# Kernel optimization log

Measured on AMD Instinct MI355X. Metric: run time of the kernel, lower is better.

## Reference

```python
import jax, jax.numpy as jnp
import numpy as np

D_MODEL = 2048
D_STATE = 16
D_CONV = 4
EXPAND = 2
D_INNER = EXPAND * D_MODEL  # 4096
BATCH = 32768


def setup_inputs() -> dict:
    key = jax.random.key(0)
    ks = jax.random.split(key, 8)
    x = jax.random.normal(ks[0], (BATCH, D_MODEL), dtype=jnp.float32)
    in_w = jax.random.normal(ks[1], (D_MODEL, D_INNER), dtype=jnp.float32) * 0.02
    in_b = jnp.zeros((D_INNER,), jnp.float32)
    # depthwise conv kernel: (d_inner, d_conv) (groups == channels, so in-chan dim is 1)
    conv_w = jax.random.normal(ks[2], (D_INNER, D_CONV), dtype=jnp.float32) * 0.1
    conv_b = jnp.zeros((D_INNER,), jnp.float32)
    # A = log(arange(1, d_state+1)) broadcast to (d_inner, d_state), as in __init__
    A_log = jnp.log(jnp.broadcast_to(
        jnp.arange(1, D_STATE + 1, dtype=jnp.float32), (D_INNER, D_STATE)))
    B = jax.random.normal(ks[3], (D_INNER, D_STATE), dtype=jnp.float32)
    C = jax.random.normal(ks[4], (D_INNER, D_STATE), dtype=jnp.float32)
    Dp = jnp.ones((D_INNER,), jnp.float32)
    dt = jnp.ones((D_INNER,), jnp.float32)
    out_w = jax.random.normal(ks[5], (D_INNER, D_MODEL), dtype=jnp.float32) * 0.02
    out_b = jnp.zeros((D_MODEL,), jnp.float32)
    return dict(x=x, in_w=in_w, in_b=in_b, conv_w=conv_w, conv_b=conv_b,
                A_log=A_log, B=B, C=C, Dp=Dp, dt=dt, out_w=out_w, out_b=out_b)


def reference(x, in_w, in_b, conv_w, conv_b, A_log, B, C, Dp, dt, out_w, out_b):
    # in_proj: (batch, d_model) -> (batch, d_inner)
    xi = x @ in_w + in_b

    # Depthwise causal Conv1d(kernel=d_conv, padding=d_conv-1) on a length-1
    # sequence; torch takes x_conv[:, :, :1]. Output position 0 sees (d_conv-1)
    # left-pad zeros followed by x, so only the LAST kernel tap contributes:
    x_conv = xi * conv_w[:, -1] + conv_b  # (batch, d_inner)

    # Single-step selective scan with zero initial state:
    #   delta = softplus(dt);  A = -exp(A_log)
    #   h = exp(delta*A) * h0 + delta * B * u  (h0 = 0 => exp term vanishes)
    #   y = sum_n C[:,n] * h[:,:,n] + D * u
    # which reduces per-channel to: y = u * (delta * sum_n(B*C) + D)
    delta = jax.nn.softplus(dt)                       # (d_inner,)
    A = -jnp.exp(A_log)                               # (d_inner, d_state) (cancels with h0=0)
    del A
    bc = jnp.sum(B * C, axis=-1)                      # (d_inner,)
    y = xi * (delta * bc + Dp)                        # (batch, d_inner)

    out = jax.nn.silu(x_conv + y)                     # SiLU gate
    return out @ out_w + out_b                        # (batch, d_model)
```

## Files before the change

kernel.cpp:

```cpp
#include <hip/hip_runtime.h>
#include <stdint.h>
#include <stddef.h>

#define D_MODEL 2048
#define D_INNER 4096

typedef float f32x4 __attribute__((ext_vector_type(4)));
typedef short short8 __attribute__((ext_vector_type(8)));
typedef __bf16 bf16x8 __attribute__((ext_vector_type(8)));

static __device__ __forceinline__ unsigned short f32_to_bf16(float f){
  unsigned int u = __builtin_bit_cast(unsigned int, f);
  u += 0x7FFFu + ((u >> 16) & 1u);
  return (unsigned short)(u >> 16);
}

static __device__ __forceinline__ f32x4 mfma_bf16(short8 a, short8 b, f32x4 c){
  return __builtin_amdgcn_mfma_f32_16x16x32_bf16(
      __builtin_bit_cast(bf16x8, a), __builtin_bit_cast(bf16x8, b), c, 0, 0, 0);
}

static __device__ __forceinline__ void gload_lds16(const void* g, void* l){
  __builtin_amdgcn_global_load_lds(
      (const __attribute__((address_space(1))) void*)g,
      (__attribute__((address_space(3))) void*)l, 16, 0, 0);
}

__global__ void prep_coef_k(const float* __restrict__ conv_w, const float* __restrict__ Bm,
                            const float* __restrict__ Cm, const float* __restrict__ Dp,
                            const float* __restrict__ dt, float* __restrict__ coef){
  int c = blockIdx.x * 256 + threadIdx.x;
  if (c >= D_INNER) return;
  float d = dt[c];
  float sp = (d > 20.f) ? d : log1pf(__expf(d));
  float bc = 0.f;
  #pragma unroll
  for (int n = 0; n < 16; n++) bc += Bm[c*16+n] * Cm[c*16+n];
  coef[c] = conv_w[c*4+3] + sp * bc + Dp[c];
}

__global__ void transpose_cvt_k(const float* __restrict__ in, unsigned short* __restrict__ outT,
                                int K, int N){
  __shared__ float t[32][33];
  int n0 = blockIdx.x * 32, k0 = blockIdx.y * 32;
  int tx = threadIdx.x, ty = threadIdx.y;
  #pragma unroll
  for (int i = 0; i < 4; i++)
    t[ty + 8*i][tx] = in[(size_t)(k0 + ty + 8*i) * N + n0 + tx];
  __syncthreads();
  #pragma unroll
  for (int i = 0; i < 4; i++)
    outT[(size_t)(n0 + ty + 8*i) * K + k0 + tx] = f32_to_bf16(t[tx][ty + 8*i]);
}

__global__ void cvt_x_k(const float4* __restrict__ x, ushort4* __restrict__ xb, int n4){
  int stride = gridDim.x * blockDim.x;
  for (int i = blockIdx.x * blockDim.x + threadIdx.x; i < n4; i += stride){
    float4 v = x[i];
    ushort4 o;
    o.x = f32_to_bf16(v.x); o.y = f32_to_bf16(v.y);
    o.z = f32_to_bf16(v.z); o.w = f32_to_bf16(v.w);
    xb[i] = o;
  }
}

template<int EPI>
__global__ __launch_bounds__(512, 2) void gemm8_k(
    const unsigned short* __restrict__ A,
    const unsigned short* __restrict__ Bt,
    int M, int N, int K,
    const float* __restrict__ bias,
    const float* __restrict__ coef,
    const float* __restrict__ convb,
    unsigned short* __restrict__ gate,
    float* __restrict__ out)
{
  __shared__ __align__(16) unsigned short smem[65536];
  char* ldsc = (char*)smem;

  const int tid = threadIdx.x;
  const int wid = tid >> 6, lane = tid & 63;
  const int wr = wid >> 2, wc = wid & 3;
  const int l15 = lane & 15, lg = lane >> 4;

  const int nbx = N >> 8;
  const int cpx = gridDim.x >> 3;
  const int bid = blockIdx.x;
  const int swz = (bid & 7) * cpx + (bid >> 3);
  const int m0 = (swz / nbx) << 8, n0 = (swz % nbx) << 8;

  const int cswz = lg ^ ((l15 >> 1) & 3);
  const int aoff = (wr*128 + l15)*64 + cswz*16;
  const int boff = (wc*64  + l15)*64 + cswz*16;

  const int s0 = wid*128 + lane;
  const int s1 = s0 + 64;
  const int r0 = s0 >> 2, r1 = s1 >> 2;
  const int c0 = (s0 & 3) ^ ((r0 >> 1) & 3);
  const int c1 = (s1 & 3) ^ ((r1 >> 1) & 3);
  const unsigned short* pA0 = A  + (size_t)(m0 + r0)*K + c0*8;
  const unsigned short* pA1 = A  + (size_t)(m0 + r1)*K + c1*8;
  const unsigned short* pB0 = Bt + (size_t)(n0 + r0)*K + c0*8;
  const unsigned short* pB1 = Bt + (size_t)(n0 + r1)*K + c1*8;

  const int ntile = K >> 6;

#define STAGE_(ST, SKS, SMAT) do {                                          \
    int st_ = (ST); if (st_ > ntile-1) st_ = ntile-1;                       \
    const int ktks_ = st_*64 + (SKS)*32;                                    \
    unsigned short* reg_ = smem + ((st_ & 1) << 15) + ((SMAT) << 14) + ((SKS) << 13); \
    if ((SMAT) == 0) {                                                      \
      gload_lds16(pA0 + ktks_, reg_ + s0*8);                                \
      gload_lds16(pA1 + ktks_, reg_ + s1*8);                                \
    } else {                                                                \
      gload_lds16(pB0 + ktks_, reg_ + s0*8);                                \
      gload_lds16(pB1 + ktks_, reg_ + s1*8);                                \
    }                                                                       \
  } while(0)

  f32x4 acc[8][4];
  #pragma unroll
  for (int i = 0; i < 8; i++)
    #pragma unroll
    for (int j = 0; j < 4; j++)
      #pragma unroll
      for (int r = 0; r < 4; r++) acc[i][j][r] = 0.f;
  short8 af[8];

  STAGE_(0,0,0); STAGE_(0,0,1); STAGE_(0,1,0); STAGE_(0,1,1);
  STAGE_(1,0,0); STAGE_(1,0,1);
  asm volatile("s_waitcnt vmcnt(4)" ::: "memory");
  __builtin_amdgcn_s_barrier();

#define CPHASE_(H, KS, NP, SMAT, SKS, TADD, DOVM) do {                      \
    const char* regA_ = ldsc + (H)*65536 + (KS)*16384;                      \
    const char* regB_ = regA_ + 32768;                                      \
    if ((NP) == 0) {                                                        \
      _Pragma("unroll")                                                     \
      for (int mi_ = 0; mi_ < 8; ++mi_)                                     \
        af[mi_] = *(const short8*)(regA_ + aoff + mi_*1024);                \
    }                                                                       \
    const short8 b0_ = *(const short8*)(regB_ + boff + (NP)*2048);          \
    const short8 b1_ = *(const short8*)(regB_ + boff + (NP)*2048 + 1024);   \
    STAGE_(t + (TADD) + (H), SKS, SMAT);                                    \
    __builtin_amdgcn_s_barrier();                                           \
    asm volatile("s_waitcnt lgkmcnt(0)" ::: "memory");                      \
    __builtin_amdgcn_sched_barrier(0);                                      \
    __builtin_amdgcn_s_setprio(1);                                          \
    _Pragma("unroll")                                                       \
    for (int mi_ = 0; mi_ < 8; ++mi_) {                                     \
      acc[mi_][(NP)*2]   = mfma_bf16(af[mi_], b0_, acc[mi_][(NP)*2]);       \
      acc[mi_][(NP)*2+1] = mfma_bf16(af[mi_], b1_, acc[mi_][(NP)*2+1]);     \
    }                                                                       \
    __builtin_amdgcn_s_setprio(0);                                          \
    if (DOVM) { asm volatile("s_waitcnt vmcnt(4)" ::: "memory"); }          \
    __builtin_amdgcn_s_barrier();                                           \
  } while(0)

  const int niter = ntile >> 1;
  #pragma unroll 1
  for (int it = 0; it < niter; ++it) {
    const int t = it << 1;
    CPHASE_(0, 0, 0, 0, 1, 1, 0);
    CPHASE_(0, 0, 1, 1, 1, 1, 0);
    CPHASE_(0, 1, 0, 0, 0, 2, 0);
    CPHASE_(0, 1, 1, 1, 0, 2, 1);
    CPHASE_(1, 0, 0, 0, 1, 1, 0);
    CPHASE_(1, 0, 1, 1, 1, 1, 0);
    CPHASE_(1, 1, 0, 0, 0, 2, 0);
    CPHASE_(1, 1, 1, 1, 0, 2, 1);
  }
#undef CPHASE_
#undef STAGE_

  const int lrow = lg << 2;
  if (EPI == 0){
    #pragma unroll
    for (int ni = 0; ni < 4; ++ni){
      const int col = n0 + wc*64 + ni*16 + l15;
      const float ib = bias[col], cf = coef[col], cb = convb[col];
      #pragma unroll
      for (int mi = 0; mi < 8; ++mi){
        const int rb = m0 + wr*128 + mi*16 + lrow;
        #pragma unroll
        for (int r = 0; r < 4; ++r){
          float z = (acc[mi][ni][r] + ib) * cf + cb;
          float g = z / (1.f + __expf(-z));
          gate[(size_t)(rb + r) * N + col] = f32_to_bf16(g);
        }
      }
    }
  } else {
    #pragma unroll
    for (int ni = 0; ni < 4; ++ni){
      const int col = n0 + wc*64 + ni*16 + l15;
      const float ob = bias[col];
      #pragma unroll
      for (int mi = 0; mi < 8; ++mi){
        const int rb = m0 + wr*128 + mi*16 + lrow;
        #pragma unroll
        for (int r = 0; r < 4; ++r)
          out[(size_t)(rb + r) * N + col] = acc[mi][ni][r] + ob;
      }
    }
  }
}

#define BM 128
#define BN 128
#define BK 64

__global__ __launch_bounds__(256) void gemm_bt_f32a_k(
    const float* __restrict__ A32, const unsigned short* __restrict__ Bt,
    int M, int N, int K,
    const float* __restrict__ bias,
    const float* __restrict__ coef,
    const float* __restrict__ convb,
    unsigned short* __restrict__ gate)
{
  __shared__ __align__(16) unsigned short lsA[BM*BK];
  __shared__ __align__(16) unsigned short lsB[BN*BK];
  const int tid = threadIdx.x;
  const int wid = tid >> 6, lane = tid & 63;
  const int wr = wid >> 1, wc = wid & 1;
  const int nbx = N / BN;
  const int cpx = gridDim.x >> 3;
  const int bid = blockIdx.x;
  const int swz = (bid & 7) * cpx + (bid >> 3);
  const int m0 = (swz / nbx) * BM, n0 = (swz % nbx) * BN;

  f32x4 acc[4][4];
  #pragma unroll
  for (int i = 0; i < 4; i++)
    #pragma unroll
    for (int j = 0; j < 4; j++)
      #pragma unroll
      for (int r = 0; r < 4; r++) acc[i][j][r] = 0.f;

  for (int kt = 0; kt < K; kt += BK){
    __syncthreads();
    #pragma unroll
    for (int i = 0; i < 8; i++){
      int c = tid + i*256;
      int row = c >> 4, c4 = (c & 15) << 2;
      const float4 v = *(const float4*)&A32[(size_t)(m0+row)*K + kt + c4];
      ushort4 o;
      o.x = f32_to_bf16(v.x); o.y = f32_to_bf16(v.y);
      o.z = f32_to_bf16(v.z); o.w = f32_to_bf16(v.w);
      *(ushort4*)&lsA[row*BK + c4] = o;
    }
    #pragma unroll
    for (int i = 0; i < 4; i++){
      int c = (wid*4 + i)*64 + lane;
      int row = c >> 3, c8 = (c & 7) << 3;
      gload_lds16(&Bt[(size_t)(n0+row)*K + kt + c8], &lsB[c*8]);
    }
    __syncthreads();

    #pragma unroll
    for (int ks = 0; ks < 2; ks++){
      short8 af[4], bf[4];
      const int ko = ks*32 + ((lane >> 4) << 3);
      #pragma unroll
      for (int mi = 0; mi < 4; mi++)
        af[mi] = *(const short8*)&lsA[(wr*64 + mi*16 + (lane & 15))*BK + ko];
      #pragma unroll
      for (int ni = 0; ni < 4; ni++)
        bf[ni] = *(const short8*)&lsB[(wc*64 + ni*16 + (lane & 15))*BK + ko];
      #pragma unroll
      for (int mi = 0; mi < 4; mi++)
        #pragma unroll
        for (int ni = 0; ni < 4; ni++)
          acc[mi][ni] = mfma_bf16(af[mi], bf[ni], acc[mi][ni]);
    }
  }

  const int lrow = (lane >> 4) << 2;
  const int lcol = lane & 15;
  #pragma unroll
  for (int ni = 0; ni < 4; ni++){
    int col = n0 + wc*64 + ni*16 + lcol;
    float ib = bias[col], cf = coef[col], cb = convb[col];
    #pragma unroll
    for (int mi = 0; mi < 4; mi++){
      int rb = m0 + wr*64 + mi*16 + lrow;
      #pragma unroll
      for (int r = 0; r < 4; r++){
        float z = (acc[mi][ni][r] + ib) * cf + cb;
        float g = z / (1.f + __expf(-z));
        gate[(size_t)(rb + r) * N + col] = f32_to_bf16(g);
      }
    }
  }
}

extern "C" void kernel_launch(void* const* d_in, const int* in_sizes, int n_in,
                              void* d_out, int out_size, void* d_ws, size_t ws_size,
                              hipStream_t stream){
  const float* x      = (const float*)d_in[0];
  const float* in_w   = (const float*)d_in[1];
  const float* in_b   = (const float*)d_in[2];
  const float* conv_w = (const float*)d_in[3];
  const float* conv_b = (const float*)d_in[4];
  const float* Bm     = (const float*)d_in[6];
  const float* Cm     = (const float*)d_in[7];
  const float* Dp     = (const float*)d_in[8];
  const float* dt     = (const float*)d_in[9];
  const float* out_w  = (const float*)d_in[10];
  const float* out_b  = (const float*)d_in[11];

  const int M = in_sizes[0] / D_MODEL;

  char* ws = (char*)d_ws;
  const size_t gate_sz = (size_t)M * D_INNER * 2;
  const size_t w1t_off = gate_sz;
  const size_t w1t_sz  = (size_t)D_MODEL * D_INNER * 2;
  const size_t w2t_off = w1t_off + w1t_sz;
  const size_t w2t_sz  = (size_t)D_INNER * D_MODEL * 2;
  const size_t coef_off = w2t_off + w2t_sz;
  const size_t coef_sz  = (size_t)D_INNER * 4;
  const size_t xb_off   = (coef_off + coef_sz + 255) & ~(size_t)255;
  const size_t xb_sz    = (size_t)M * D_MODEL * 2;

  unsigned short* gate = (unsigned short*)ws;
  unsigned short* w1t  = (unsigned short*)(ws + w1t_off);
  unsigned short* w2t  = (unsigned short*)(ws + w2t_off);
  float*          coef = (float*)(ws + coef_off);
  unsigned short* xb   = (unsigned short*)(ws + xb_off);
  const bool have_xb = ws_size >= xb_off + xb_sz;

  prep_coef_k<<<D_INNER/256, 256, 0, stream>>>(conv_w, Bm, Cm, Dp, dt, coef);
  transpose_cvt_k<<<dim3(D_INNER/32, D_MODEL/32), dim3(32,8), 0, stream>>>(in_w, w1t, D_MODEL, D_INNER);
  transpose_cvt_k<<<dim3(D_MODEL/32, D_INNER/32), dim3(32,8), 0, stream>>>(out_w, w2t, D_INNER, D_MODEL);
  if (have_xb)
    cvt_x_k<<<2048, 256, 0, stream>>>((const float4*)x, (ushort4*)xb, (M*D_MODEL)/4);

  if (have_xb){
    const int g1 = (M/256) * (D_INNER/256);
    gemm8_k<0><<<g1, 512, 0, stream>>>(xb, w1t, M, D_INNER, D_MODEL,
                                       in_b, coef, conv_b, gate, nullptr);
  } else {
    const int g1 = (M/BM) * (D_INNER/BN);
    gemm_bt_f32a_k<<<g1, 256, 0, stream>>>(x, w1t, M, D_INNER, D_MODEL,
                                           in_b, coef, conv_b, gate);
  }

  const int g2 = (M/256) * (D_MODEL/256);
  gemm8_k<1><<<g2, 512, 0, stream>>>(gate, w2t, M, D_MODEL, D_INNER,
                                     out_b, nullptr, nullptr, nullptr, (float*)d_out);
}
```

Baseline: 1.164 ms.

## Stage GEMM epilogue through LDS for coalesced vector stores; drop lgkmcnt wait

The epilogue of the 256x256 tile GEMM now writes results into LDS in passes, one half of the warps at a time, then reads back rows and issues 16-byte coalesced global stores. Before, each lane scattered 2- or 4-byte stores along columns. The explicit lgkmcnt(0) wait and sched_barrier before the MFMA block are also removed, leaving the compiler to insert LDS waits. This adds barriers and LDS round trips to the epilogue, and relies on the compiler to keep operand reads ordered correctly.

```diff
diff --git a/kernel.cpp b/kernel.cpp
--- a/kernel.cpp
+++ b/kernel.cpp
@@ -25,6 +25,10 @@
       (const __attribute__((address_space(1))) void*)g,
       (__attribute__((address_space(3))) void*)l, 16, 0, 0);
 }
+
+#define BARF() do { asm volatile("" ::: "memory"); \
+                    __builtin_amdgcn_s_barrier();  \
+                    asm volatile("" ::: "memory"); } while(0)
 
 __global__ void prep_coef_k(const float* __restrict__ conv_w, const float* __restrict__ Bm,
                             const float* __restrict__ Cm, const float* __restrict__ Dp,
@@ -144,8 +148,6 @@
     const short8 b1_ = *(const short8*)(regB_ + boff + (NP)*2048 + 1024);   \
     STAGE_(t + (TADD) + (H), SKS, SMAT);                                    \
     __builtin_amdgcn_s_barrier();                                           \
-    asm volatile("s_waitcnt lgkmcnt(0)" ::: "memory");                      \
-    __builtin_amdgcn_sched_barrier(0);                                      \
     __builtin_amdgcn_s_setprio(1);                                          \
     _Pragma("unroll")                                                       \
     for (int mi_ = 0; mi_ < 8; ++mi_) {                                     \
@@ -173,35 +175,70 @@
 #undef CPHASE_
 #undef STAGE_
 
+  asm volatile("s_waitcnt vmcnt(0)" ::: "memory");
+  BARF();
+
   const int lrow = lg << 2;
   if (EPI == 0){
-    #pragma unroll
-    for (int ni = 0; ni < 4; ++ni){
-      const int col = n0 + wc*64 + ni*16 + l15;
-      const float ib = bias[col], cf = coef[col], cb = convb[col];
-      #pragma unroll
-      for (int mi = 0; mi < 8; ++mi){
-        const int rb = m0 + wr*128 + mi*16 + lrow;
+    unsigned short* st = smem;
+    #pragma unroll 1
+    for (int p = 0; p < 2; ++p){
+      if (wr == p){
         #pragma unroll
-        for (int r = 0; r < 4; ++r){
-          float z = (acc[mi][ni][r] + ib) * cf + cb;
-          float g = z / (1.f + __expf(-z));
-          gate[(size_t)(rb + r) * N + col] = f32_to_bf16(g);
+        for (int ni = 0; ni < 4; ++ni){
+          const int col = wc*64 + ni*16 + l15;
+          const int gcol = n0 + col;
+          const float ib = bias[gcol], cf = coef[gcol], cb = convb[gcol];
+          #pragma unroll
+          for (int mi = 0; mi < 8; ++mi){
+            const int rl = mi*16 + lrow;
+            #pragma unroll
+            for (int r = 0; r < 4; ++r){
+              float z = (acc[mi][ni][r] + ib) * cf + cb;
+              float g = z / (1.f + __expf(-z));
+              st[(rl + r)*264 + col] = f32_to_bf16(g);
+            }
+          }
         }
       }
+      BARF();
+      #pragma unroll
+      for (int rd = 0; rd < 8; ++rd){
+        const int idx = rd*512 + tid;
+        const int row = idx >> 5, c8 = (idx & 31) << 3;
+        short8 v = *(const short8*)&st[row*264 + c8];
+        *(short8*)&gate[(size_t)(m0 + p*128 + row) * N + n0 + c8] = v;
+      }
+      BARF();
     }
   } else {
-    #pragma unroll
-    for (int ni = 0; ni < 4; ++ni){
-      const int col = n0 + wc*64 + ni*16 + l15;
-      const float ob = bias[col];
-      #pragma unroll
-      for (int mi = 0; mi < 8; ++mi){
-        const int rb = m0 + wr*128 + mi*16 + lrow;
+    float* stf = (float*)smem;
+    #pragma unroll 1
+    for (int p = 0; p < 4; ++p){
+      if (wr == (p >> 1)){
         #pragma unroll
-        for (int r = 0; r < 4; ++r)
-          out[(size_t)(rb + r) * N + col] = acc[mi][ni][r] + ob;
-      }
+        for (int ni = 0; ni < 4; ++ni){
+          const int col = wc*64 + ni*16 + l15;
+          const float ob = bias[n0 + col];
+          #pragma unroll
+          for (int mi2 = 0; mi2 < 4; ++mi2){
+            const int mi = (p & 1)*4 + mi2;
+            const int rl = mi2*16 + lrow;
+            #pragma unroll
+            for (int r = 0; r < 4; ++r)
+              stf[(rl + r)*260 + col] = acc[mi][ni][r] + ob;
+          }
+        }
+      }
+      BARF();
+      #pragma unroll
+      for (int rd = 0; rd < 8; ++rd){
+        const int idx = rd*512 + tid;
+        const int row = idx >> 6, c4 = (idx & 63) << 2;
+        f32x4 v = *(const f32x4*)&stf[row*260 + c4];
+        *(f32x4*)&out[(size_t)(m0 + p*64 + row) * N + n0 + c4] = v;
+      }
+      BARF();
     }
   }
 }
```

After: 1.271 ms. 9.2% more time.
